# Kernel tuning notes

Measured on AMD Instinct MI355X. Metric: run time of the kernel, lower is better.

The kernel has to match this reference:

```python
import jax, jax.numpy as jnp
import numpy as np

B, T, C, H = 2, 2048, 1024, 16
HS = C // H  # 64
EPS = 1e-5


def layer_norm(x, w, b):
    mu = jnp.mean(x, axis=-1, keepdims=True)
    var = jnp.var(x, axis=-1, keepdims=True)
    return (x - mu) * jax.lax.rsqrt(var + EPS) * w + b


def setup_inputs() -> dict:
    key = jax.random.key(0)
    ks = jax.random.split(key, 16)
    s_c = 1.0 / np.sqrt(C)
    s_f = 1.0 / np.sqrt(4 * C)
    u = lambda k, shape, s: jax.random.uniform(k, shape, jnp.float32, -s, s)
    return {
        "x": jax.random.normal(ks[0], (B, T, C), jnp.float32),
        # per-head Q/K/V Linears stacked over heads: [H, C, HS], bias [H, HS]
        "Wq": u(ks[1], (H, C, HS), s_c), "bq": u(ks[2], (H, HS), s_c),
        "Wk": u(ks[3], (H, C, HS), s_c), "bk": u(ks[4], (H, HS), s_c),
        "Wv": u(ks[5], (H, C, HS), s_c), "bv": u(ks[6], (H, HS), s_c),
        "Wp": u(ks[7], (C, C), s_c), "bp": u(ks[8], (C,), s_c),
        "W1": u(ks[9], (C, 4 * C), s_c), "b1": u(ks[10], (4 * C,), s_c),
        "W2": u(ks[11], (4 * C, C), s_f), "b2": u(ks[12], (C,), s_f),
        "ln1_w": jnp.ones((C,), jnp.float32), "ln1_b": jnp.zeros((C,), jnp.float32),
        "ln2_w": jnp.ones((C,), jnp.float32), "ln2_b": jnp.zeros((C,), jnp.float32),
    }


def reference(x, Wq, bq, Wk, bk, Wv, bv, Wp, bp, W1, b1, W2, b2,
              ln1_w, ln1_b, ln2_w, ln2_b):
    # --- pre-norm self-attention ---
    xn = layer_norm(x, ln1_w, ln1_b)
    q = jnp.einsum('btc,hcd->bhtd', xn, Wq) + bq[None, :, None, :]
    k = jnp.einsum('btc,hcd->bhtd', xn, Wk) + bk[None, :, None, :]
    v = jnp.einsum('btc,hcd->bhtd', xn, Wv) + bv[None, :, None, :]
    # NOTE: original scales by C**-0.5 (full embedding dim), not head_size**-0.5
    att = jnp.einsum('bhtd,bhsd->bhts', q, k) * (C ** -0.5)
    att = jax.nn.softmax(att, axis=-1)
    o = jnp.einsum('bhts,bhsd->bhtd', att, v)  # [B,H,T,HS]
    o = jnp.transpose(o, (0, 2, 1, 3)).reshape(B, T, C)  # concat heads
    sa = o @ Wp + bp
    out = x + sa
    # --- pre-norm FFN (exact erf GELU, matching nn.GELU default) ---
    on = layer_norm(out, ln2_w, ln2_b)
    h = jax.nn.gelu(on @ W1 + b1, approximate=False)
    return out + (h @ W2 + b2)
```

## Files before the change

kernel.cpp:

```cpp
#include <hip/hip_runtime.h>
#include <math.h>

#define BB 2
#define TT 2048
#define CC 1024
#define HH 16
#define HS 64
#define MT 4096
#define FF 4096

typedef unsigned short u16;
typedef __bf16 bfrag __attribute__((ext_vector_type(8)));
typedef float f4 __attribute__((ext_vector_type(4)));

#define AS1(p) ((const __attribute__((address_space(1))) void*)(p))
#define AS3(p) ((__attribute__((address_space(3))) void*)(p))

__device__ __forceinline__ u16 f2bf(float f) {
  union { float f; unsigned u; } a; a.f = f;
  return (u16)((a.u + 0x7fffu + ((a.u >> 16) & 1u)) >> 16);
}

__device__ __forceinline__ int swz128(int byteoff) {
  return byteoff ^ (((byteoff >> 7) & 7) << 4);
}

__device__ __forceinline__ int swzAB(int byteoff) {
  return byteoff ^ (((byteoff >> 7) & 3) << 4);
}

__global__ void tr_f32_bf16(const float* __restrict__ src, u16* __restrict__ dst,
                            int R, int Cc, long long sb, long long db, int dld) {
  __shared__ float t[32][33];
  const int bz = blockIdx.z;
  const int r0 = blockIdx.y * 32, c0 = blockIdx.x * 32;
  const int tx = threadIdx.x, ty = threadIdx.y;
  const float* s = src + bz * sb;
  u16* d = dst + bz * db;
#pragma unroll
  for (int i = 0; i < 4; i++)
    t[ty + i * 8][tx] = s[(size_t)(r0 + ty + i * 8) * Cc + c0 + tx];
  __syncthreads();
#pragma unroll
  for (int i = 0; i < 4; i++)
    d[(size_t)(c0 + ty + i * 8) * dld + r0 + tx] = f2bf(t[tx][ty + i * 8]);
}

__global__ void tr_bf16(const u16* __restrict__ src, u16* __restrict__ dst,
                        int R, int Cc, long long sb, long long db, int dld) {
  __shared__ u16 t[32][33];
  const int bz = blockIdx.z;
  const int r0 = blockIdx.y * 32, c0 = blockIdx.x * 32;
  const int tx = threadIdx.x, ty = threadIdx.y;
  const u16* s = src + bz * sb;
  u16* d = dst + bz * db;
#pragma unroll
  for (int i = 0; i < 4; i++)
    t[ty + i * 8][tx] = s[(size_t)(r0 + ty + i * 8) * Cc + c0 + tx];
  __syncthreads();
#pragma unroll
  for (int i = 0; i < 4; i++)
    d[(size_t)(c0 + ty + i * 8) * dld + r0 + tx] = t[tx][ty + i * 8];
}

__global__ __launch_bounds__(256) void ln_kernel(
    const float* __restrict__ x, const float* __restrict__ w,
    const float* __restrict__ b, u16* __restrict__ y) {
  const int row = blockIdx.x, tid = threadIdx.x;
  const float4 v = reinterpret_cast<const float4*>(x + (size_t)row * CC)[tid];
  float s = v.x + v.y + v.z + v.w;
  float s2 = v.x * v.x + v.y * v.y + v.z * v.z + v.w * v.w;
#pragma unroll
  for (int off = 32; off >= 1; off >>= 1) {
    s += __shfl_xor(s, off);
    s2 += __shfl_xor(s2, off);
  }
  __shared__ float ps[4], ps2[4];
  const int wave = tid >> 6, lane = tid & 63;
  if (lane == 0) { ps[wave] = s; ps2[wave] = s2; }
  __syncthreads();
  s = ps[0] + ps[1] + ps[2] + ps[3];
  s2 = ps2[0] + ps2[1] + ps2[2] + ps2[3];
  const float mu = s * (1.f / CC);
  const float rstd = rsqrtf(s2 * (1.f / CC) - mu * mu + 1e-5f);
  const float4 wv = reinterpret_cast<const float4*>(w)[tid];
  const float4 bv = reinterpret_cast<const float4*>(b)[tid];
  ushort4 o;
  o.x = f2bf((v.x - mu) * rstd * wv.x + bv.x);
  o.y = f2bf((v.y - mu) * rstd * wv.y + bv.y);
  o.z = f2bf((v.z - mu) * rstd * wv.z + bv.z);
  o.w = f2bf((v.w - mu) * rstd * wv.w + bv.w);
  reinterpret_cast<ushort4*>(y + (size_t)row * CC)[tid] = o;
}

template<int NJ>
__device__ __forceinline__ void gemm_core(
    const u16* __restrict__ A, const u16* __restrict__ Bt, int K,
    f4 (&acc)[4][NJ]) {
  constexpr int BN = NJ * 32;
  __shared__ u16 As[3][128 * 32];
  __shared__ u16 Bs[3][BN * 32];
  const int tid = threadIdx.x;
  const int wave = tid >> 6, lane = tid & 63;
  const int wm = wave >> 1, wn = wave & 1;
  const int lg = lane >> 4, ll = lane & 15;

  const int trow = tid >> 2;
  const int tch  = (tid & 3) ^ ((trow >> 1) & 3);
  const u16* ga = A + (size_t)(blockIdx.y * 128 + trow) * K + tch * 8;
  const u16* gb = Bt + (size_t)(blockIdx.x * BN + trow) * K + tch * 8;
  const size_t g64 = (size_t)64 * K;
  const int nt = K >> 5;

  auto GSTAGE = [&](int bi, int kt) {
    u16* la = &As[bi][tid * 8];
    u16* lb = &Bs[bi][tid * 8];
    const u16* gA = ga + kt * 32;
    const u16* gB = gb + kt * 32;
    __builtin_amdgcn_global_load_lds(AS1(gA), AS3(la), 16, 0, 0);
    __builtin_amdgcn_global_load_lds(AS1(gA + g64), AS3(la + 2048), 16, 0, 0);
    __builtin_amdgcn_global_load_lds(AS1(gB), AS3(lb), 16, 0, 0);
    if constexpr (NJ == 4)
      __builtin_amdgcn_global_load_lds(AS1(gB + g64), AS3(lb + 2048), 16, 0, 0);
  };

  GSTAGE(0, 0);
  GSTAGE(1, 1);
  GSTAGE(2, 2);
  int bi = 0;
  for (int t = 0; t < nt; t++) {
    const int ahead = nt - 1 - t;
    if constexpr (NJ == 4) {
      if (ahead >= 2)      asm volatile("s_waitcnt vmcnt(8)" ::: "memory");
      else if (ahead == 1) asm volatile("s_waitcnt vmcnt(4)" ::: "memory");
      else                 asm volatile("s_waitcnt vmcnt(0)" ::: "memory");
    } else {
      if (ahead >= 2)      asm volatile("s_waitcnt vmcnt(6)" ::: "memory");
      else if (ahead == 1) asm volatile("s_waitcnt vmcnt(3)" ::: "memory");
      else                 asm volatile("s_waitcnt vmcnt(0)" ::: "memory");
    }
    __builtin_amdgcn_s_barrier();
    __builtin_amdgcn_sched_barrier(0);

    const char* as_ = (const char*)As[bi];
    const char* bs_ = (const char*)Bs[bi];
    bfrag af[4], bf[NJ];
#pragma unroll
    for (int i = 0; i < 4; i++)
      af[i] = *(const bfrag*)(as_ + swzAB((wm * 64 + i * 16 + ll) * 64 + lg * 16));
#pragma unroll
    for (int j = 0; j < NJ; j++)
      bf[j] = *(const bfrag*)(bs_ + swzAB((wn * (BN / 2) + j * 16 + ll) * 64 + lg * 16));

    __builtin_amdgcn_s_setprio(1);
#pragma unroll
    for (int i = 0; i < 4; i++)
#pragma unroll
      for (int j = 0; j < NJ; j++)
        acc[i][j] = __builtin_amdgcn_mfma_f32_16x16x32_bf16(af[i], bf[j], acc[i][j], 0, 0, 0);
    __builtin_amdgcn_s_setprio(0);

    __builtin_amdgcn_sched_barrier(0);
    __builtin_amdgcn_s_barrier();
    if (t + 3 < nt) GSTAGE(bi, t + 3);
    bi = (bi == 2) ? 0 : bi + 1;
  }
}

#define EPI_COORDS                                              \
  const int tid = threadIdx.x;                                  \
  const int wave = tid >> 6, lane = tid & 63;                   \
  const int wm = wave >> 1, wn = wave & 1;                      \
  const int lg = lane >> 4, ll = lane & 15;

__global__ __launch_bounds__(256, 2) void gemm_qkv(
    const u16* __restrict__ A, const u16* __restrict__ Bt,
    const float* __restrict__ bq, const float* __restrict__ bk,
    const float* __restrict__ bv,
    u16* __restrict__ q, u16* __restrict__ k, u16* __restrict__ v) {
  f4 acc[4][4] = {};
  gemm_core<4>(A, Bt, CC, acc);
  EPI_COORDS
#pragma unroll
  for (int j = 0; j < 4; j++) {
    const int n = blockIdx.x * 128 + wn * 64 + j * 16 + ll;
    const int sec = n >> 10, nn = n & 1023, h = nn >> 6, d = nn & 63;
    const float bias = (sec == 0 ? bq : (sec == 1 ? bk : bv))[nn];
    const float scale = (sec == 0) ? 0.03125f : 1.0f;
    u16* dst = sec == 0 ? q : (sec == 1 ? k : v);
#pragma unroll
    for (int i = 0; i < 4; i++)
#pragma unroll
      for (int r = 0; r < 4; r++) {
        const int m = blockIdx.y * 128 + wm * 64 + i * 16 + lg * 4 + r;
        const int b = m >> 11, t = m & 2047;
        dst[(((size_t)b * HH + h) * TT + t) * HS + d] = f2bf((acc[i][j][r] + bias) * scale);
      }
  }
}

__global__ __launch_bounds__(256, 2) void gemm_proj(
    const u16* __restrict__ A, const u16* __restrict__ Bt,
    const float* __restrict__ bp, const float* __restrict__ x,
    float* __restrict__ outw) {
  f4 acc[4][2] = {};
  gemm_core<2>(A, Bt, CC, acc);
  EPI_COORDS
#pragma unroll
  for (int i = 0; i < 4; i++)
#pragma unroll
    for (int j = 0; j < 2; j++) {
      const int n = blockIdx.x * 64 + wn * 32 + j * 16 + ll;
      const float bias = bp[n];
#pragma unroll
      for (int r = 0; r < 4; r++) {
        const int m = blockIdx.y * 128 + wm * 64 + i * 16 + lg * 4 + r;
        const size_t idx = (size_t)m * CC + n;
        outw[idx] = acc[i][j][r] + bias + x[idx];
      }
    }
}

__global__ __launch_bounds__(256, 2) void gemm_ffn1(
    const u16* __restrict__ A, const u16* __restrict__ Bt,
    const float* __restrict__ b1, u16* __restrict__ hb) {
  f4 acc[4][4] = {};
  gemm_core<4>(A, Bt, CC, acc);
  EPI_COORDS
#pragma unroll
  for (int i = 0; i < 4; i++)
#pragma unroll
    for (int j = 0; j < 4; j++) {
      const int n = blockIdx.x * 128 + wn * 64 + j * 16 + ll;
      const float bias = b1[n];
#pragma unroll
      for (int r = 0; r < 4; r++) {
        const int m = blockIdx.y * 128 + wm * 64 + i * 16 + lg * 4 + r;
        const float t = acc[i][j][r] + bias;
        const float g = 0.5f * t * (1.0f + erff(t * 0.70710678118654752f));
        hb[(size_t)m * FF + n] = f2bf(g);
      }
    }
}

__global__ __launch_bounds__(256, 2) void gemm_ffn2(
    const u16* __restrict__ A, const u16* __restrict__ Bt,
    const float* __restrict__ b2, const float* __restrict__ outw,
    float* __restrict__ dout) {
  f4 acc[4][2] = {};
  gemm_core<2>(A, Bt, FF, acc);
  EPI_COORDS
#pragma unroll
  for (int i = 0; i < 4; i++)
#pragma unroll
    for (int j = 0; j < 2; j++) {
      const int n = blockIdx.x * 64 + wn * 32 + j * 16 + ll;
      const float bias = b2[n];
#pragma unroll
      for (int r = 0; r < 4; r++) {
        const int m = blockIdx.y * 128 + wm * 64 + i * 16 + lg * 4 + r;
        const size_t idx = (size_t)m * CC + n;
        dout[idx] = acc[i][j][r] + bias + outw[idx];
      }
    }
}

__global__ __launch_bounds__(256, 2) void attn_kernel(
    const u16* __restrict__ Q, const u16* __restrict__ Kb,
    const u16* __restrict__ Vt, u16* __restrict__ Ao) {
  __shared__ __align__(1024) u16 Ks[2][64 * 64];
  __shared__ __align__(1024) u16 Vs[2][64 * 64];
  __shared__ __align__(1024) u16 Ps[4][32 * 64];
  const int bh = blockIdx.y, qt = blockIdx.x;
  const int tid = threadIdx.x, wave = tid >> 6, lane = tid & 63;
  const int lg = lane >> 4, ll = lane & 15;

  bfrag qf[2][2];
  const u16* Qb = Q + ((size_t)bh * TT + qt * 128 + wave * 32) * HS;
#pragma unroll
  for (int qb = 0; qb < 2; qb++)
#pragma unroll
    for (int dc = 0; dc < 2; dc++)
      qf[qb][dc] = *(const bfrag*)&Qb[(qb * 16 + ll) * HS + dc * 32 + lg * 8];

  f4 o[2][4] = {};
  float mrun[2] = {-INFINITY, -INFINITY}, lrun[2] = {0.f, 0.f};

  const int trow = tid >> 3;
  const int tch  = (tid & 7) ^ (trow & 7);
  const u16* gk = Kb + ((size_t)bh * TT + trow) * HS + tch * 8;
  const u16* gv = Vt + ((size_t)bh * HS + trow) * TT + tch * 8;

  char* const pw = (char*)Ps[wave];

#define STAGE(bufi, stt)                                                          \
  do {                                                                            \
    u16* lk = &Ks[bufi][tid * 8];                                                 \
    u16* lv = &Vs[bufi][tid * 8];                                                 \
    __builtin_amdgcn_global_load_lds(AS1(gk + (size_t)(stt) * HS), AS3(lk), 16, 0, 0); \
    __builtin_amdgcn_global_load_lds(AS1(gk + (size_t)(stt) * HS + 32 * HS), AS3(lk + 2048), 16, 0, 0); \
    __builtin_amdgcn_global_load_lds(AS1(gv + (stt)), AS3(lv), 16, 0, 0);         \
    __builtin_amdgcn_global_load_lds(AS1(gv + (stt) + (size_t)32 * TT), AS3(lv + 2048), 16, 0, 0); \
  } while (0)

  STAGE(0, 0);
  int cur = 0;

  for (int st = 0; st < TT; st += 64) {
    if (st + 64 < TT) {
      STAGE(cur ^ 1, st + 64);
      asm volatile("s_waitcnt vmcnt(4)" ::: "memory");
    } else {
      asm volatile("s_waitcnt vmcnt(0)" ::: "memory");
    }
    __builtin_amdgcn_s_barrier();
    __builtin_amdgcn_sched_barrier(0);

    const char* kbuf = (const char*)Ks[cur];
    const char* vbuf = (const char*)Vs[cur];

    f4 p[2][4];
#pragma unroll
    for (int kb = 0; kb < 4; kb++) {
      const int row = kb * 16 + ll;
      const bfrag k0 = *(const bfrag*)(kbuf + swz128(row * 128 + lg * 16));
      const bfrag k1 = *(const bfrag*)(kbuf + swz128(row * 128 + 64 + lg * 16));
#pragma unroll
      for (int qb = 0; qb < 2; qb++) {
        f4 z = {0.f, 0.f, 0.f, 0.f};
        z = __builtin_amdgcn_mfma_f32_16x16x32_bf16(k0, qf[qb][0], z, 0, 0, 0);
        p[qb][kb] = __builtin_amdgcn_mfma_f32_16x16x32_bf16(k1, qf[qb][1], z, 0, 0, 0);
      }
    }

#pragma unroll
    for (int qb = 0; qb < 2; qb++) {
      float pm = p[qb][0][0];
#pragma unroll
      for (int kb = 0; kb < 4; kb++)
#pragma unroll
        for (int r = 0; r < 4; r++)
          if (kb | r) pm = fmaxf(pm, p[qb][kb][r]);
      pm = fmaxf(pm, __shfl_xor(pm, 16));
      pm = fmaxf(pm, __shfl_xor(pm, 32));
      const float mn = fmaxf(mrun[qb], pm);
      const float al = __expf(mrun[qb] - mn);
      mrun[qb] = mn;
      float rs = 0.f;
#pragma unroll
      for (int kb = 0; kb < 4; kb++)
#pragma unroll
        for (int r = 0; r < 4; r++) {
          const float e = __expf(p[qb][kb][r] - mn);
          p[qb][kb][r] = e;
          rs += e;
        }
      rs += __shfl_xor(rs, 16);
      rs += __shfl_xor(rs, 32);
      lrun[qb] = lrun[qb] * al + rs;
#pragma unroll
      for (int fo = 0; fo < 4; fo++) o[qb][fo] *= al;
#pragma unroll
      for (int kb = 0; kb < 4; kb++) {
        union { uint2 v; __bf16 h[4]; } w;
        w.h[0] = (__bf16)p[qb][kb][0];
        w.h[1] = (__bf16)p[qb][kb][1];
        w.h[2] = (__bf16)p[qb][kb][2];
        w.h[3] = (__bf16)p[qb][kb][3];
        *(uint2*)(pw + swz128((qb * 16 + ll) * 128 + kb * 32 + lg * 8)) = w.v;
      }
    }

#pragma unroll
    for (int ks = 0; ks < 2; ks++) {
      const bfrag pb0 = *(const bfrag*)(pw + swz128(ll * 128 + ks * 64 + lg * 16));
      const bfrag pb1 = *(const bfrag*)(pw + swz128((16 + ll) * 128 + ks * 64 + lg * 16));
#pragma unroll
      for (int fo = 0; fo < 4; fo++) {
        const bfrag vf = *(const bfrag*)(vbuf + swz128((fo * 16 + ll) * 128 + ks * 64 + lg * 16));
        o[0][fo] = __builtin_amdgcn_mfma_f32_16x16x32_bf16(vf, pb0, o[0][fo], 0, 0, 0);
        o[1][fo] = __builtin_amdgcn_mfma_f32_16x16x32_bf16(vf, pb1, o[1][fo], 0, 0, 0);
      }
    }

    __builtin_amdgcn_sched_barrier(0);
    __builtin_amdgcn_s_barrier();
    cur ^= 1;
  }
#undef STAGE

  const int b = bh >> 4, h = bh & 15;
#pragma unroll
  for (int qb = 0; qb < 2; qb++) {
    const float inv = 1.0f / lrun[qb];
    const int t = qt * 128 + wave * 32 + qb * 16 + ll;
#pragma unroll
    for (int fo = 0; fo < 4; fo++) {
      union { uint2 v; __bf16 h[4]; } w;
      w.h[0] = (__bf16)(o[qb][fo][0] * inv);
      w.h[1] = (__bf16)(o[qb][fo][1] * inv);
      w.h[2] = (__bf16)(o[qb][fo][2] * inv);
      w.h[3] = (__bf16)(o[qb][fo][3] * inv);
      *(uint2*)&Ao[((size_t)b * TT + t) * CC + h * HS + fo * 16 + lg * 4] = w.v;
    }
  }
}

extern "C" void kernel_launch(void* const* d_in, const int* in_sizes, int n_in,
                              void* d_out, int out_size, void* d_ws, size_t ws_size,
                              hipStream_t stream) {
  const float* x    = (const float*)d_in[0];
  const float* Wq   = (const float*)d_in[1];
  const float* bq   = (const float*)d_in[2];
  const float* Wk   = (const float*)d_in[3];
  const float* bk   = (const float*)d_in[4];
  const float* Wv   = (const float*)d_in[5];
  const float* bv   = (const float*)d_in[6];
  const float* Wp   = (const float*)d_in[7];
  const float* bp   = (const float*)d_in[8];
  const float* W1   = (const float*)d_in[9];
  const float* b1   = (const float*)d_in[10];
  const float* W2   = (const float*)d_in[11];
  const float* b2   = (const float*)d_in[12];
  const float* ln1w = (const float*)d_in[13];
  const float* ln1b = (const float*)d_in[14];
  const float* ln2w = (const float*)d_in[15];
  const float* ln2b = (const float*)d_in[16];
  float* dout = (float*)d_out;

  char* ws = (char*)d_ws;
  u16* wqkv = (u16*)(ws + 0);
  u16* wpt  = (u16*)(ws + 6291456);
  u16* w1t  = (u16*)(ws + 8388608);
  u16* w2t  = (u16*)(ws + 16777216);
  u16* xn   = (u16*)(ws + 25165824);
  u16* qb   = (u16*)(ws + 33554432);
  u16* kb   = (u16*)(ws + 41943040);
  u16* vb   = (u16*)(ws + 50331648);
  u16* vt   = (u16*)(ws + 58720256);
  u16* ao   = (u16*)(ws + 67108864);
  u16* hb   = qb;

  dim3 blk256(256);
  dim3 blkT(32, 8);

  tr_f32_bf16<<<dim3(2, 32, 16), blkT, 0, stream>>>(Wq, wqkv,               1024,   64, 65536LL, 65536LL, 1024);
  tr_f32_bf16<<<dim3(2, 32, 16), blkT, 0, stream>>>(Wk, wqkv + 1024 * 1024, 1024,   64, 65536LL, 65536LL, 1024);
  tr_f32_bf16<<<dim3(2, 32, 16), blkT, 0, stream>>>(Wv, wqkv + 2048 * 1024, 1024,   64, 65536LL, 65536LL, 1024);
  tr_f32_bf16<<<dim3(32, 32, 1),  blkT, 0, stream>>>(Wp, wpt, 1024, 1024, 0LL, 0LL, 1024);
  tr_f32_bf16<<<dim3(128, 32, 1), blkT, 0, stream>>>(W1, w1t, 1024, 4096, 0LL, 0LL, 1024);
  tr_f32_bf16<<<dim3(32, 128, 1), blkT, 0, stream>>>(W2, w2t, 4096, 1024, 0LL, 0LL, 4096);

  ln_kernel<<<dim3(MT), blk256, 0, stream>>>(x, ln1w, ln1b, xn);

  gemm_qkv<<<dim3(24, 32), blk256, 0, stream>>>(xn, wqkv, bq, bk, bv, qb, kb, vb);

  tr_bf16<<<dim3(2, 64, 32), blkT, 0, stream>>>(vb, vt, 2048, 64, 131072LL, 131072LL, 2048);

  attn_kernel<<<dim3(16, 32), blk256, 0, stream>>>(qb, kb, vt, ao);

  gemm_proj<<<dim3(16, 32), blk256, 0, stream>>>(ao, wpt, bp, x, dout);

  ln_kernel<<<dim3(MT), blk256, 0, stream>>>(dout, ln2w, ln2b, xn);

  gemm_ffn1<<<dim3(32, 32), blk256, 0, stream>>>(xn, w1t, b1, hb);
  gemm_ffn2<<<dim3(16, 32), blk256, 0, stream>>>(hb, w2t, b2, dout, dout);
}
```

Before: 292.0 us.

## Use 256x256-tile 512-thread GEMM core for QKV and FFN1 projections

Adds a new GEMM core with 256x256 output tiles, eight waves per block, a K-step of 64 and double-buffered LDS staging through direct global-to-LDS loads. The QKV and FFN1 kernels move onto it, with their launch grids shrunk to match. The goal is to raise arithmetic intensity per block and cut global and L2 traffic for the two largest-N GEMMs. In exchange, each block uses about 128 KB of LDS and 128 accumulator registers per thread, so only one block fits per CU. The QKV grid also drops to 192 blocks, which may leave some CUs idle.

```diff
diff --git a/kernel.cpp b/kernel.cpp
--- a/kernel.cpp
+++ b/kernel.cpp
@@ -93,6 +93,146 @@
   reinterpret_cast<ushort4*>(y + (size_t)row * CC)[tid] = o;
 }
 
+__device__ __forceinline__ void gemm256_core(
+    const u16* __restrict__ A, const u16* __restrict__ Bt, int K,
+    f4 (&acc)[8][4]) {
+  __shared__ u16 As[2][256 * 64];
+  __shared__ u16 Bs[2][256 * 64];
+  const int tid = threadIdx.x;
+  const int wave = tid >> 6, lane = tid & 63;
+  const int wm = wave >> 2, wn = wave & 3;
+  const int lg = lane >> 4, ll = lane & 15;
+
+  const int trow = tid >> 3;
+  const int tch  = (tid & 7) ^ (trow & 7);
+  const u16* ga = A + (size_t)(blockIdx.y * 256 + trow) * K + tch * 8;
+  const u16* gb = Bt + (size_t)(blockIdx.x * 256 + trow) * K + tch * 8;
+  const size_t gs = (size_t)64 * K;
+  const int nt = K >> 6;
+
+  auto STAGE = [&](int bi, int kt) {
+    u16* la = &As[bi][tid * 8];
+    u16* lb = &Bs[bi][tid * 8];
+    const u16* gA = ga + kt * 64;
+    const u16* gB = gb + kt * 64;
+#pragma unroll
+    for (int j = 0; j < 4; j++)
+      __builtin_amdgcn_global_load_lds(AS1(gA + j * gs), AS3(la + j * 4096), 16, 0, 0);
+#pragma unroll
+    for (int j = 0; j < 4; j++)
+      __builtin_amdgcn_global_load_lds(AS1(gB + j * gs), AS3(lb + j * 4096), 16, 0, 0);
+  };
+
+  STAGE(0, 0);
+  int cur = 0;
+  for (int t = 0; t < nt; t++) {
+    if (t + 1 < nt) {
+      STAGE(cur ^ 1, t + 1);
+      asm volatile("s_waitcnt vmcnt(8)" ::: "memory");
+    } else {
+      asm volatile("s_waitcnt vmcnt(0)" ::: "memory");
+    }
+    __builtin_amdgcn_s_barrier();
+    __builtin_amdgcn_sched_barrier(0);
+
+    const char* as_ = (const char*)As[cur];
+    const char* bs_ = (const char*)Bs[cur];
+
+#pragma unroll
+    for (int kh = 0; kh < 2; kh++) {
+      bfrag bf[4], af[4];
+#pragma unroll
+      for (int j = 0; j < 4; j++)
+        bf[j] = *(const bfrag*)(bs_ + swz128((wn * 64 + j * 16 + ll) * 128 + kh * 64 + lg * 16));
+#pragma unroll
+      for (int i = 0; i < 4; i++)
+        af[i] = *(const bfrag*)(as_ + swz128((wm * 128 + i * 16 + ll) * 128 + kh * 64 + lg * 16));
+      __builtin_amdgcn_s_barrier();
+      asm volatile("s_waitcnt lgkmcnt(0)" ::: "memory");
+      __builtin_amdgcn_sched_barrier(0);
+      __builtin_amdgcn_s_setprio(1);
+#pragma unroll
+      for (int i = 0; i < 4; i++)
+#pragma unroll
+        for (int j = 0; j < 4; j++)
+          acc[i][j] = __builtin_amdgcn_mfma_f32_16x16x32_bf16(af[i], bf[j], acc[i][j], 0, 0, 0);
+      __builtin_amdgcn_s_setprio(0);
+      __builtin_amdgcn_sched_barrier(0);
+      __builtin_amdgcn_s_barrier();
+#pragma unroll
+      for (int i = 0; i < 4; i++)
+        af[i] = *(const bfrag*)(as_ + swz128((wm * 128 + 64 + i * 16 + ll) * 128 + kh * 64 + lg * 16));
+      __builtin_amdgcn_s_barrier();
+      asm volatile("s_waitcnt lgkmcnt(0)" ::: "memory");
+      __builtin_amdgcn_sched_barrier(0);
+      __builtin_amdgcn_s_setprio(1);
+#pragma unroll
+      for (int i = 0; i < 4; i++)
+#pragma unroll
+        for (int j = 0; j < 4; j++)
+          acc[4 + i][j] = __builtin_amdgcn_mfma_f32_16x16x32_bf16(af[i], bf[j], acc[4 + i][j], 0, 0, 0);
+      __builtin_amdgcn_s_setprio(0);
+      __builtin_amdgcn_sched_barrier(0);
+      __builtin_amdgcn_s_barrier();
+    }
+    cur ^= 1;
+  }
+}
+
+__global__ __launch_bounds__(512, 2) void gemm_qkv(
+    const u16* __restrict__ A, const u16* __restrict__ Bt,
+    const float* __restrict__ bq, const float* __restrict__ bk,
+    const float* __restrict__ bv,
+    u16* __restrict__ q, u16* __restrict__ k, u16* __restrict__ v) {
+  f4 acc[8][4] = {};
+  gemm256_core(A, Bt, CC, acc);
+  const int tid = threadIdx.x;
+  const int wave = tid >> 6, lane = tid & 63;
+  const int wm = wave >> 2, wn = wave & 3;
+  const int lg = lane >> 4, ll = lane & 15;
+#pragma unroll
+  for (int j = 0; j < 4; j++) {
+    const int n = blockIdx.x * 256 + wn * 64 + j * 16 + ll;
+    const int sec = n >> 10, nn = n & 1023, h = nn >> 6, d = nn & 63;
+    const float bias = (sec == 0 ? bq : (sec == 1 ? bk : bv))[nn];
+    const float scale = (sec == 0) ? 0.03125f : 1.0f;
+    u16* dst = sec == 0 ? q : (sec == 1 ? k : v);
+#pragma unroll
+    for (int i = 0; i < 8; i++)
+#pragma unroll
+      for (int r = 0; r < 4; r++) {
+        const int m = blockIdx.y * 256 + wm * 128 + i * 16 + lg * 4 + r;
+        const int b = m >> 11, t = m & 2047;
+        dst[(((size_t)b * HH + h) * TT + t) * HS + d] = f2bf((acc[i][j][r] + bias) * scale);
+      }
+  }
+}
+
+__global__ __launch_bounds__(512, 2) void gemm_ffn1(
+    const u16* __restrict__ A, const u16* __restrict__ Bt,
+    const float* __restrict__ b1, u16* __restrict__ hb) {
+  f4 acc[8][4] = {};
+  gemm256_core(A, Bt, CC, acc);
+  const int tid = threadIdx.x;
+  const int wave = tid >> 6, lane = tid & 63;
+  const int wm = wave >> 2, wn = wave & 3;
+  const int lg = lane >> 4, ll = lane & 15;
+#pragma unroll
+  for (int j = 0; j < 4; j++) {
+    const int n = blockIdx.x * 256 + wn * 64 + j * 16 + ll;
+    const float bias = b1[n];
+#pragma unroll
+    for (int i = 0; i < 8; i++)
+#pragma unroll
+      for (int r = 0; r < 4; r++) {
+        const int m = blockIdx.y * 256 + wm * 128 + i * 16 + lg * 4 + r;
+        const float t = acc[i][j][r] + bias;
+        const float g = 0.5f * t * (1.0f + erff(t * 0.70710678118654752f));
+        hb[(size_t)m * FF + n] = f2bf(g);
+      }
+  }
+}
+
 template<int NJ>
 __device__ __forceinline__ void gemm_core(
     const u16* __restrict__ A, const u16* __restrict__ Bt, int K,
@@ -173,32 +313,6 @@
   const int wm = wave >> 1, wn = wave & 1;                      \
   const int lg = lane >> 4, ll = lane & 15;
 
-__global__ __launch_bounds__(256, 2) void gemm_qkv(
-    const u16* __restrict__ A, const u16* __restrict__ Bt,
-    const float* __restrict__ bq, const float* __restrict__ bk,
-    const float* __restrict__ bv,
-    u16* __restrict__ q, u16* __restrict__ k, u16* __restrict__ v) {
-  f4 acc[4][4] = {};
-  gemm_core<4>(A, Bt, CC, acc);
-  EPI_COORDS
-#pragma unroll
-  for (int j = 0; j < 4; j++) {
-    const int n = blockIdx.x * 128 + wn * 64 + j * 16 + ll;
-    const int sec = n >> 10, nn = n & 1023, h = nn >> 6, d = nn & 63;
-    const float bias = (sec == 0 ? bq : (sec == 1 ? bk : bv))[nn];
-    const float scale = (sec == 0) ? 0.03125f : 1.0f;
-    u16* dst = sec == 0 ? q : (sec == 1 ? k : v);
-#pragma unroll
-    for (int i = 0; i < 4; i++)
-#pragma unroll
-      for (int r = 0; r < 4; r++) {
-        const int m = blockIdx.y * 128 + wm * 64 + i * 16 + lg * 4 + r;
-        const int b = m >> 11, t = m & 2047;
-        dst[(((size_t)b * HH + h) * TT + t) * HS + d] = f2bf((acc[i][j][r] + bias) * scale);
-      }
-  }
-}
-
 __global__ __launch_bounds__(256, 2) void gemm_proj(
     const u16* __restrict__ A, const u16* __restrict__ Bt,
     const float* __restrict__ bp, const float* __restrict__ x,
@@ -217,28 +331,6 @@
         const int m = blockIdx.y * 128 + wm * 64 + i * 16 + lg * 4 + r;
         const size_t idx = (size_t)m * CC + n;
         outw[idx] = acc[i][j][r] + bias + x[idx];
-      }
-    }
-}
-
-__global__ __launch_bounds__(256, 2) void gemm_ffn1(
-    const u16* __restrict__ A, const u16* __restrict__ Bt,
-    const float* __restrict__ b1, u16* __restrict__ hb) {
-  f4 acc[4][4] = {};
-  gemm_core<4>(A, Bt, CC, acc);
-  EPI_COORDS
-#pragma unroll
-  for (int i = 0; i < 4; i++)
-#pragma unroll
-    for (int j = 0; j < 4; j++) {
-      const int n = blockIdx.x * 128 + wn * 64 + j * 16 + ll;
-      const float bias = b1[n];
-#pragma unroll
-      for (int r = 0; r < 4; r++) {
-        const int m = blockIdx.y * 128 + wm * 64 + i * 16 + lg * 4 + r;
-        const float t = acc[i][j][r] + bias;
-        const float g = 0.5f * t * (1.0f + erff(t * 0.70710678118654752f));
-        hb[(size_t)m * FF + n] = f2bf(g);
       }
     }
 }
@@ -442,6 +534,7 @@
   u16* hb   = qb;
 
   dim3 blk256(256);
+  dim3 blk512(512);
   dim3 blkT(32, 8);
 
   tr_f32_bf16<<<dim3(2, 32, 16), blkT, 0, stream>>>(Wq, wqkv,               1024,   64, 65536LL, 65536LL, 1024);
@@ -453,7 +546,7 @@
 
   ln_kernel<<<dim3(MT), blk256, 0, stream>>>(x, ln1w, ln1b, xn);
 
-  gemm_qkv<<<dim3(24, 32), blk256, 0, stream>>>(xn, wqkv, bq, bk, bv, qb, kb, vb);
+  gemm_qkv<<<dim3(12, 16), blk512, 0, stream>>>(xn, wqkv, bq, bk, bv, qb, kb, vb);
 
   tr_bf16<<<dim3(2, 64, 32), blkT, 0, stream>>>(vb, vt, 2048, 64, 131072LL, 131072LL, 2048);
 
@@ -463,6 +556,6 @@
 
   ln_kernel<<<dim3(MT), blk256, 0, stream>>>(dout, ln2w, ln2b, xn);
 
-  gemm_ffn1<<<dim3(32, 32), blk256, 0, stream>>>(xn, w1t, b1, hb);
+  gemm_ffn1<<<dim3(16, 16), blk512, 0, stream>>>(xn, w1t, b1, hb);
   gemm_ffn2<<<dim3(16, 32), blk256, 0, stream>>>(hb, w2t, b2, dout, dout);
 }
```

Measured after the change: 300.3 us. +2.8%, slower.
